# Kernel optimization log

Hardware: AMD Instinct MI355X
Metric: run time of the kernel (lower is better)

## Reference

```python
import jax, jax.numpy as jnp
import numpy as np

N = 500_000   # mesh vertices
M = 500_000   # non-manifold sample points
K = 4         # quad-mesh valence
WEIGHTS = [7000.0, 600.0, 10.0, 50.0, 30.0, 3.0]


def setup_inputs() -> dict:
    key = jax.random.key(0)
    ks = jax.random.split(key, 11)
    return {
        "manifold_pred": jax.random.normal(ks[0], (1, N), jnp.float32),
        "nonmanifold_pred": jax.random.normal(ks[1], (1, M), jnp.float32),
        "mnfld_grad": jax.random.normal(ks[2], (1, N, 3), jnp.float32),
        "nonmnfld_grad": jax.random.normal(ks[3], (1, M, 3), jnp.float32),
        "mnfld_hessian": jax.random.normal(ks[4], (1, N, 3, 3), jnp.float32),
        "mnfld_n_gt": jax.random.normal(ks[5], (1, N, 3), jnp.float32),
        "theta": jax.random.normal(ks[6], (1, N, 1), jnp.float32),
        "local_coord_u": jax.random.normal(ks[7], (1, N, 3), jnp.float32),
        "local_coord_v": jax.random.normal(ks[8], (1, N, 3), jnp.float32),
        "rot": jax.random.normal(ks[9], (N, K, 3, 3), jnp.float32),
        "neighbors": jax.random.randint(ks[10], (N, K), 0, N, jnp.int32),
    }


def reference(manifold_pred, nonmanifold_pred, mnfld_grad, nonmnfld_grad,
              mnfld_hessian, mnfld_n_gt, theta, local_coord_u, local_coord_v,
              rot, neighbors):
    H = mnfld_hessian[0]          # [N,3,3] per-vertex hessian
    n_gt = mnfld_n_gt[0]          # [N,3]

    # morse term: n^T H  (div_type == 'l1')
    morse = 0.5 * jnp.abs(jnp.einsum('nd,nde->ne', n_gt, H)).mean()

    sdf_term = jnp.abs(manifold_pred).mean()

    # eikonal over concatenated grads (morse path uses nonmnfld_grad when near_points is None)
    all_grads = jnp.concatenate([nonmnfld_grad, mnfld_grad], axis=-2)  # [1, M+N, 3]
    eikonal_term = jnp.abs(jnp.linalg.norm(all_grads, axis=2) - 1.0).mean()

    inter_term = jnp.exp(-100.0 * jnp.abs(nonmanifold_pred)).mean()

    # cross-field directions from theta
    u, v, th = local_coord_u[0], local_coord_v[0], theta[0]  # [N,3],[N,3],[N,1]
    va = u * jnp.cos(th) + v * jnp.sin(th)
    va = va / (jnp.linalg.norm(va, axis=-1, keepdims=True) + 1e-12)
    vb = -u * jnp.sin(th) + v * jnp.cos(th)
    vb = vb / (jnp.linalg.norm(vb, axis=-1, keepdims=True) + 1e-12)

    # per-vertex (v^T H) x v hessian alignment (single valence group covers all vertices)
    vaH = jnp.einsum('nd,nde->ne', va, H)
    vbH = jnp.einsum('nd,nde->ne', vb, H)
    h_alpha = jnp.abs(jnp.cross(vaH, va)).mean()
    h_beta = jnp.abs(jnp.cross(vbH, vb)).mean()
    theta_hessian_term = 0.5 * (h_alpha + h_beta)

    # neighbor consistency: rotate neighbor cross-field into vertex frame, dot products
    vaj = jnp.einsum('nkij,nkj->nki', rot, va[neighbors])  # [N,K,3]
    vbj = jnp.einsum('nkij,nkj->nki', rot, vb[neighbors])
    aa = jnp.abs(jnp.einsum('nd,nkd->nk', va, vaj))
    ab = jnp.abs(jnp.einsum('nd,nkd->nk', va, vbj))
    ba = jnp.abs(jnp.einsum('nd,nkd->nk', vb, vaj))
    bb = jnp.abs(jnp.einsum('nd,nkd->nk', vb, vbj))
    theta_neighbors_term = (aa + ab + ba + bb - 2.0).mean()

    w = WEIGHTS
    loss = (w[0] * sdf_term + w[1] * inter_term + w[3] * eikonal_term
            + w[5] * morse + w[2] * theta_hessian_term + w[4] * theta_neighbors_term)
    return jnp.stack([loss, sdf_term, inter_term, eikonal_term, morse,
                      theta_hessian_term, theta_neighbors_term])
```

## Files before the change

### kernel.cpp

```cpp
#include <hip/hip_runtime.h>
#include <math.h>

static constexpr int BLOCK = 256;
static constexpr int WAVES = BLOCK / 64;
static constexpr int KVAL = 4;
static constexpr int TILE = 256;

typedef float f4 __attribute__((ext_vector_type(4)));
typedef int i4 __attribute__((ext_vector_type(4)));
typedef unsigned int u4v __attribute__((ext_vector_type(4)));
union VV { u4v u4; _Float16 h[8]; };

__device__ __forceinline__ void nts4(u4v* p, u4v v) {
  __builtin_nontemporal_store(v, p);
}

__device__ __forceinline__ void norm3(float x, float y, float z,
                                      float& ox, float& oy, float& oz) {
  float inv = 1.0f / (sqrtf(x * x + y * y + z * z) + 1e-12f);
  ox = x * inv; oy = y * inv; oz = z * inv;
}

template <int NV>
__device__ __forceinline__ void block_reduce(float (&p)[NV]) {
#pragma unroll
  for (int off = 32; off > 0; off >>= 1)
#pragma unroll
    for (int q = 0; q < NV; ++q) p[q] += __shfl_down(p[q], off, 64);
  __shared__ float sm[WAVES][NV];
  int wave = threadIdx.x >> 6, lane = threadIdx.x & 63;
  if (lane == 0)
#pragma unroll
    for (int q = 0; q < NV; ++q) sm[wave][q] = p[q];
  __syncthreads();
  if (threadIdx.x == 0) {
#pragma unroll
    for (int q = 0; q < NV; ++q) {
      float t = 0.f;
#pragma unroll
      for (int w = 1; w < WAVES; ++w) t += sm[w][q];
      p[q] += t;
    }
  }
}

__device__ __forceinline__ void stage_f(float* __restrict__ dst,
                                        const float* __restrict__ src, int nf) {
  int t = threadIdx.x;
  int nf4 = nf >> 2;
  const f4* s4 = (const f4*)src;
  f4* d4 = (f4*)dst;
  for (int i = t; i < nf4; i += BLOCK) d4[i] = s4[i];
  int rem = nf & 3;
  if (t < rem) dst[nf4 * 4 + t] = src[nf4 * 4 + t];
}

__global__ __launch_bounds__(BLOCK) void s1_kernel(
    const float* __restrict__ theta, const float* __restrict__ u,
    const float* __restrict__ v, u4v* __restrict__ vavb, int N,
    const float* __restrict__ pred, const float* __restrict__ pgrad,
    const float* __restrict__ mp, const float* __restrict__ grad,
    const float* __restrict__ H, const float* __restrict__ ngt,
    float* __restrict__ part1, int nb1, int M) {
  __shared__ float B[2304];
  int t = threadIdx.x;
  long base = (long)blockIdx.x * TILE;
  float p[5] = {0.f, 0.f, 0.f, 0.f, 0.f};

  int cntM = 0, cntN = 0;
  if (base < M) { long c = (long)M - base; cntM = c > TILE ? TILE : (int)c; }
  if (base < N) { long c = (long)N - base; cntN = c > TILE ? TILE : (int)c; }

  float prv = 0.f, mpv = 0.f, thv = 0.f;
  if (t < cntM) prv = pred[base + t];
  if (t < cntN) { mpv = mp[base + t]; thv = theta[base + t]; }

  if (cntM > 0) stage_f(B, pgrad + 3 * base, 3 * cntM);
  __syncthreads();
  if (t < cntM) {
    float gx = B[3 * t], gy = B[3 * t + 1], gz = B[3 * t + 2];
    p[1] += fabsf(sqrtf(gx * gx + gy * gy + gz * gz) - 1.0f);
    p[4] += __expf(-100.0f * fabsf(prv));
  }
  __syncthreads();
  float ng0 = 0.f, ng1 = 0.f, ng2 = 0.f;
  if (cntN > 0) {
    stage_f(B, grad + 3 * base, 3 * cntN);
    stage_f(B + 768, ngt + 3 * base, 3 * cntN);
  }
  __syncthreads();
  if (t < cntN) {
    float gx = B[3 * t], gy = B[3 * t + 1], gz = B[3 * t + 2];
    p[1] += fabsf(sqrtf(gx * gx + gy * gy + gz * gz) - 1.0f);
    p[0] = fabsf(mpv);
    ng0 = B[768 + 3 * t]; ng1 = B[768 + 3 * t + 1]; ng2 = B[768 + 3 * t + 2];
  }
  __syncthreads();

  if (cntN > 0) {
    stage_f(B, u + 3 * base, 3 * cntN);
    stage_f(B + 768, v + 3 * base, 3 * cntN);
  }
  __syncthreads();
  float va[3] = {0.f, 0.f, 0.f}, vb[3] = {0.f, 0.f, 0.f};
  if (t < cntN) {
    float s, c;
    __sincosf(thv, &s, &c);
    float ux = B[3 * t], uy = B[3 * t + 1], uz = B[3 * t + 2];
    float vx = B[768 + 3 * t], vy = B[768 + 3 * t + 1], vz = B[768 + 3 * t + 2];
    norm3(ux * c + vx * s, uy * c + vy * s, uz * c + vz * s, va[0], va[1], va[2]);
    norm3(vx * c - ux * s, vy * c - uy * s, vz * c - uz * s, vb[0], vb[1], vb[2]);
    VV o;
    o.h[0] = (_Float16)va[0]; o.h[1] = (_Float16)va[1]; o.h[2] = (_Float16)va[2];
    o.h[3] = (_Float16)vb[0]; o.h[4] = (_Float16)vb[1]; o.h[5] = (_Float16)vb[2];
    o.h[6] = (_Float16)0.f;   o.h[7] = (_Float16)0.f;
    nts4(&vavb[base + t], o.u4);
  }
  __syncthreads();

  if (cntN > 0) stage_f(B, H + 9 * base, 9 * cntN);
  __syncthreads();
  if (t < cntN) {
    float h[9];
#pragma unroll
    for (int q = 0; q < 9; ++q) h[q] = B[9 * t + q];
    p[2] = fabsf(ng0 * h[0] + ng1 * h[3] + ng2 * h[6]) +
           fabsf(ng0 * h[1] + ng1 * h[4] + ng2 * h[7]) +
           fabsf(ng0 * h[2] + ng1 * h[5] + ng2 * h[8]);
    float a0 = va[0] * h[0] + va[1] * h[3] + va[2] * h[6];
    float a1 = va[0] * h[1] + va[1] * h[4] + va[2] * h[7];
    float a2 = va[0] * h[2] + va[1] * h[5] + va[2] * h[8];
    float b0 = vb[0] * h[0] + vb[1] * h[3] + vb[2] * h[6];
    float b1 = vb[0] * h[1] + vb[1] * h[4] + vb[2] * h[7];
    float b2 = vb[0] * h[2] + vb[1] * h[5] + vb[2] * h[8];
    p[3] = fabsf(a1 * va[2] - a2 * va[1]) + fabsf(a2 * va[0] - a0 * va[2]) +
           fabsf(a0 * va[1] - a1 * va[0]) + fabsf(b1 * vb[2] - b2 * vb[1]) +
           fabsf(b2 * vb[0] - b0 * vb[2]) + fabsf(b0 * vb[1] - b1 * vb[0]);
  }

  block_reduce<5>(p);
  if (t == 0) {
#pragma unroll
    for (int q = 0; q < 5; ++q) part1[q * nb1 + blockIdx.x] = p[q];
  }
}

__global__ __launch_bounds__(BLOCK) void s3_kernel(
    const u4v* __restrict__ vavb, const float* __restrict__ rot,
    const i4* __restrict__ nbr, float* __restrict__ part2, int N) {
  __shared__ float B[4608];
  int t = threadIdx.x;
  long base = (long)blockIdx.x * TILE;
  int cntN = 0;
  if (base < N) { long c = (long)N - base; cntN = c > TILE ? TILE : (int)c; }
  float p[1] = {0.f};

  VV wn[4]; VV ws;
  ws.u4 = u4v{0, 0, 0, 0};
#pragma unroll
  for (int k = 0; k < KVAL; ++k) wn[k].u4 = u4v{0, 0, 0, 0};
  if (t < cntN) {
    i4 jj = nbr[base + t];
    int js[4] = {jj.x, jj.y, jj.z, jj.w};
#pragma unroll
    for (int k = 0; k < KVAL; ++k) wn[k].u4 = vavb[js[k]];
    ws.u4 = vavb[base + t];
  }
  float va[3] = {(float)ws.h[0], (float)ws.h[1], (float)ws.h[2]};
  float vb[3] = {(float)ws.h[3], (float)ws.h[4], (float)ws.h[5]};

  float nsum = 0.f;
#pragma unroll
  for (int sp = 0; sp < 2; ++sp) {
    int cs = cntN - 128 * sp;
    if (cs < 0) cs = 0;
    if (cs > 128) cs = 128;
    if (cs > 0) stage_f(B, rot + 36 * (base + 128 * sp), 36 * cs);
    __syncthreads();
    int lt = t - 128 * sp;
    if (lt >= 0 && lt < cs) {
      const float* R0 = B + 36 * lt;
#pragma unroll
      for (int k = 0; k < KVAL; ++k) {
        float R[9];
#pragma unroll
        for (int q = 0; q < 9; ++q) R[q] = R0[9 * k + q];
        float pa0 = R[0] * va[0] + R[3] * va[1] + R[6] * va[2];
        float pa1 = R[1] * va[0] + R[4] * va[1] + R[7] * va[2];
        float pa2 = R[2] * va[0] + R[5] * va[1] + R[8] * va[2];
        float pb0 = R[0] * vb[0] + R[3] * vb[1] + R[6] * vb[2];
        float pb1 = R[1] * vb[0] + R[4] * vb[1] + R[7] * vb[2];
        float pb2 = R[2] * vb[0] + R[5] * vb[1] + R[8] * vb[2];
        float aj0 = (float)wn[k].h[0], aj1 = (float)wn[k].h[1],
              aj2 = (float)wn[k].h[2];
        float bj0 = (float)wn[k].h[3], bj1 = (float)wn[k].h[4],
              bj2 = (float)wn[k].h[5];
        nsum += fabsf(pa0 * aj0 + pa1 * aj1 + pa2 * aj2) +
                fabsf(pa0 * bj0 + pa1 * bj1 + pa2 * bj2) +
                fabsf(pb0 * aj0 + pb1 * aj1 + pb2 * aj2) +
                fabsf(pb0 * bj0 + pb1 * bj1 + pb2 * bj2) - 2.0f;
      }
    }
    __syncthreads();
  }
  p[0] = nsum;
  block_reduce<1>(p);
  if (t == 0) part2[blockIdx.x] = p[0];
}

__global__ __launch_bounds__(BLOCK) void finalize_fast(
    const float* __restrict__ part1, int nb1, const float* __restrict__ part2,
    int nb2, float* __restrict__ out, int N, int M) {
  float s[6] = {0.f, 0.f, 0.f, 0.f, 0.f, 0.f};
  for (int b = threadIdx.x; b < nb1; b += BLOCK) {
#pragma unroll
    for (int q = 0; q < 5; ++q) s[q] += part1[q * nb1 + b];
  }
  for (int b = threadIdx.x; b < nb2; b += BLOCK) s[5] += part2[b];
  block_reduce<6>(s);
  if (threadIdx.x == 0) {
    float sdf = s[0] / (float)N;
    float eik = s[1] / (float)(N + M);
    float morse = 0.5f * s[2] / (3.0f * (float)N);
    float th = 0.5f * s[3] / (3.0f * (float)N);
    float inter = s[4] / (float)M;
    float nb = s[5] / ((float)N * (float)KVAL);
    float loss = 7000.0f * sdf + 600.0f * inter + 50.0f * eik + 3.0f * morse +
                 10.0f * th + 30.0f * nb;
    out[0] = loss; out[1] = sdf; out[2] = inter; out[3] = eik;
    out[4] = morse; out[5] = th; out[6] = nb;
  }
}

__device__ __forceinline__ void crossfield(const float* __restrict__ u,
                                           const float* __restrict__ v,
                                           const float* __restrict__ theta,
                                           int n, float va[3], float vb[3]) {
  float s, c;
  __sincosf(theta[n], &s, &c);
  float ux = u[3 * n], uy = u[3 * n + 1], uz = u[3 * n + 2];
  float vx = v[3 * n], vy = v[3 * n + 1], vz = v[3 * n + 2];
  norm3(ux * c + vx * s, uy * c + vy * s, uz * c + vz * s, va[0], va[1], va[2]);
  norm3(vx * c - ux * s, vy * c - uy * s, vz * c - uz * s, vb[0], vb[1], vb[2]);
}

__global__ __launch_bounds__(BLOCK) void vertex_kernel(
    const float* __restrict__ mp, const float* __restrict__ grad,
    const float* __restrict__ H, const float* __restrict__ ngt,
    const float* __restrict__ theta, const float* __restrict__ u,
    const float* __restrict__ v, const float* __restrict__ rot,
    const int* __restrict__ nbr, float* __restrict__ acc, int N) {
  int n = blockIdx.x * blockDim.x + threadIdx.x;
  float p[5] = {0.f, 0.f, 0.f, 0.f, 0.f};
  if (n < N) {
    float hh[9];
#pragma unroll
    for (int i = 0; i < 9; ++i) hh[i] = H[9 * (size_t)n + i];
    p[0] = fabsf(mp[n]);
    float gx = grad[3 * n], gy = grad[3 * n + 1], gz = grad[3 * n + 2];
    p[1] = fabsf(sqrtf(gx * gx + gy * gy + gz * gz) - 1.0f);
    float n0 = ngt[3 * n], n1 = ngt[3 * n + 1], n2 = ngt[3 * n + 2];
    p[2] = fabsf(n0 * hh[0] + n1 * hh[3] + n2 * hh[6]) +
           fabsf(n0 * hh[1] + n1 * hh[4] + n2 * hh[7]) +
           fabsf(n0 * hh[2] + n1 * hh[5] + n2 * hh[8]);
    float va[3], vb[3];
    crossfield(u, v, theta, n, va, vb);
    {
      float a0 = va[0] * hh[0] + va[1] * hh[3] + va[2] * hh[6];
      float a1 = va[0] * hh[1] + va[1] * hh[4] + va[2] * hh[7];
      float a2 = va[0] * hh[2] + va[1] * hh[5] + va[2] * hh[8];
      float b0 = vb[0] * hh[0] + vb[1] * hh[3] + vb[2] * hh[6];
      float b1 = vb[0] * hh[1] + vb[1] * hh[4] + vb[2] * hh[7];
      float b2 = vb[0] * hh[2] + vb[1] * hh[5] + vb[2] * hh[8];
      p[3] = fabsf(a1 * va[2] - a2 * va[1]) + fabsf(a2 * va[0] - a0 * va[2]) +
             fabsf(a0 * va[1] - a1 * va[0]) + fabsf(b1 * vb[2] - b2 * vb[1]) +
             fabsf(b2 * vb[0] - b0 * vb[2]) + fabsf(b0 * vb[1] - b1 * vb[0]);
    }
    float nsum = 0.f;
    const float* R = rot + (size_t)n * (KVAL * 9);
#pragma unroll
    for (int k = 0; k < KVAL; ++k) {
      int j = nbr[KVAL * (size_t)n + k];
      float vaj[3], vbj[3];
      crossfield(u, v, theta, j, vaj, vbj);
      float r0 = R[9 * k + 0], r1 = R[9 * k + 1], r2 = R[9 * k + 2];
      float r3 = R[9 * k + 3], r4 = R[9 * k + 4], r5 = R[9 * k + 5];
      float r6 = R[9 * k + 6], r7 = R[9 * k + 7], r8 = R[9 * k + 8];
      float wa0 = r0 * vaj[0] + r1 * vaj[1] + r2 * vaj[2];
      float wa1 = r3 * vaj[0] + r4 * vaj[1] + r5 * vaj[2];
      float wa2 = r6 * vaj[0] + r7 * vaj[1] + r8 * vaj[2];
      float wb0 = r0 * vbj[0] + r1 * vbj[1] + r2 * vbj[2];
      float wb1 = r3 * vbj[0] + r4 * vbj[1] + r5 * vbj[2];
      float wb2 = r6 * vbj[0] + r7 * vbj[1] + r8 * vbj[2];
      nsum += fabsf(va[0] * wa0 + va[1] * wa1 + va[2] * wa2) +
              fabsf(va[0] * wb0 + va[1] * wb1 + va[2] * wb2) +
              fabsf(vb[0] * wa0 + vb[1] * wa1 + vb[2] * wa2) +
              fabsf(vb[0] * wb0 + vb[1] * wb1 + vb[2] * wb2) - 2.0f;
    }
    p[4] = nsum;
  }
  block_reduce<5>(p);
  if (threadIdx.x == 0) {
    atomicAdd(&acc[0], p[0]); atomicAdd(&acc[1], p[1]); atomicAdd(&acc[2], p[2]);
    atomicAdd(&acc[3], p[3]); atomicAdd(&acc[4], p[4]);
  }
}

__global__ __launch_bounds__(BLOCK) void point_kernel(
    const float* __restrict__ pred, const float* __restrict__ grad,
    float* __restrict__ acc, int M) {
  int i = blockIdx.x * blockDim.x + threadIdx.x;
  float p[2] = {0.f, 0.f};
  if (i < M) {
    p[0] = __expf(-100.0f * fabsf(pred[i]));
    float gx = grad[3 * i], gy = grad[3 * i + 1], gz = grad[3 * i + 2];
    p[1] = fabsf(sqrtf(gx * gx + gy * gy + gz * gz) - 1.0f);
  }
  block_reduce<2>(p);
  if (threadIdx.x == 0) {
    atomicAdd(&acc[5], p[0]); atomicAdd(&acc[1], p[1]);
  }
}

__global__ void finalize_acc(const float* __restrict__ acc, float* __restrict__ out,
                             int N, int M) {
  if (threadIdx.x == 0 && blockIdx.x == 0) {
    float sdf = acc[0] / (float)N;
    float eik = acc[1] / (float)(N + M);
    float morse = 0.5f * acc[2] / (3.0f * (float)N);
    float th = 0.5f * acc[3] / (3.0f * (float)N);
    float nb = acc[4] / ((float)N * (float)KVAL);
    float inter = acc[5] / (float)M;
    float loss = 7000.0f * sdf + 600.0f * inter + 50.0f * eik + 3.0f * morse +
                 10.0f * th + 30.0f * nb;
    out[0] = loss; out[1] = sdf; out[2] = inter; out[3] = eik;
    out[4] = morse; out[5] = th; out[6] = nb;
  }
}

extern "C" void kernel_launch(void* const* d_in, const int* in_sizes, int n_in,
                              void* d_out, int out_size, void* d_ws, size_t ws_size,
                              hipStream_t stream) {
  const float* mp    = (const float*)d_in[0];
  const float* npred = (const float*)d_in[1];
  const float* grad  = (const float*)d_in[2];
  const float* ngrad = (const float*)d_in[3];
  const float* H     = (const float*)d_in[4];
  const float* ngt   = (const float*)d_in[5];
  const float* theta = (const float*)d_in[6];
  const float* u     = (const float*)d_in[7];
  const float* v     = (const float*)d_in[8];
  const float* rot   = (const float*)d_in[9];
  const int*   nbr   = (const int*)d_in[10];
  float* out = (float*)d_out;

  int N = in_sizes[0];
  int M = in_sizes[1];
  int mx = (N > M) ? N : M;
  int nb1 = (mx + TILE - 1) / TILE;
  int nb2 = (N + TILE - 1) / TILE;

  size_t off_vavb = 256;
  size_t off_p1 = off_vavb + (size_t)N * 16;
  size_t off_p2 = off_p1 + (size_t)5 * nb1 * 4;
  size_t need = off_p2 + (size_t)nb2 * 4;

  if (ws_size >= need) {
    u4v* vavb    = (u4v*)((char*)d_ws + off_vavb);
    float* part1 = (float*)((char*)d_ws + off_p1);
    float* part2 = (float*)((char*)d_ws + off_p2);
    s1_kernel<<<nb1, BLOCK, 0, stream>>>(
        theta, u, v, vavb, N, npred, ngrad, mp, grad, H, ngt, part1, nb1, M);
    s3_kernel<<<nb2, BLOCK, 0, stream>>>(
        vavb, rot, (const i4*)nbr, part2, N);
    finalize_fast<<<1, BLOCK, 0, stream>>>(part1, nb1, part2, nb2, out, N, M);
  } else {
    float* acc = (float*)d_ws;
    (void)hipMemsetAsync(acc, 0, 6 * sizeof(float), stream);
    vertex_kernel<<<(N + BLOCK - 1) / BLOCK, BLOCK, 0, stream>>>(
        mp, grad, H, ngt, theta, u, v, rot, nbr, acc, N);
    point_kernel<<<(M + BLOCK - 1) / BLOCK, BLOCK, 0, stream>>>(npred, ngrad, acc, M);
    finalize_acc<<<1, 64, 0, stream>>>(acc, out, N, M);
  }
}
```

Before: 59.84 us.

## Split each vertex's neighbors across two threads and pad staged rot rows

The neighbor-consistency kernel now assigns two threads per vertex, each handling two of the four neighbors, so both halves of the tile run compute in each staging phase instead of half the block idling. The neighbor-index and vertex-data gathers are issued up front for both sub-tiles. Rotation matrices are staged into shared memory with a 37-float stride to avoid LDS bank conflicts. The cost is more gathers per thread (the own-vertex vavb load is duplicated across the pair) and integer division in the staging loop.

After: 59.77 us. No clear change (-0.1%).

```diff
diff --git a/kernel.cpp b/kernel.cpp
--- a/kernel.cpp
+++ b/kernel.cpp
@@ -8,6 +8,7 @@
 
 typedef float f4 __attribute__((ext_vector_type(4)));
 typedef int i4 __attribute__((ext_vector_type(4)));
+typedef int i2 __attribute__((ext_vector_type(2)));
 typedef unsigned int u4v __attribute__((ext_vector_type(4)));
 union VV { u4v u4; _Float16 h[8]; };
 
@@ -53,6 +54,19 @@
   for (int i = t; i < nf4; i += BLOCK) d4[i] = s4[i];
   int rem = nf & 3;
   if (t < rem) dst[nf4 * 4 + t] = src[nf4 * 4 + t];
+}
+
+__device__ __forceinline__ void stage_rot_pad(float* __restrict__ B,
+                                              const float* __restrict__ src,
+                                              int cs) {
+  int nf4 = 9 * cs;
+  const f4* s4 = (const f4*)src;
+  for (int i = threadIdx.x; i < nf4; i += BLOCK) {
+    f4 x = s4[i];
+    int vtx = i / 9, r = i - 9 * vtx;
+    float* d = B + vtx * 37 + r * 4;
+    d[0] = x.x; d[1] = x.y; d[2] = x.z; d[3] = x.w;
+  }
 }
 
 __global__ __launch_bounds__(BLOCK) void s1_kernel(
@@ -147,27 +161,30 @@
 
 __global__ __launch_bounds__(BLOCK) void s3_kernel(
     const u4v* __restrict__ vavb, const float* __restrict__ rot,
-    const i4* __restrict__ nbr, float* __restrict__ part2, int N) {
-  __shared__ float B[4608];
+    const i2* __restrict__ nbr2, float* __restrict__ part2, int N) {
+  __shared__ float B[128 * 37];
   int t = threadIdx.x;
+  int vl = t >> 1;
+  int h = t & 1;
   long base = (long)blockIdx.x * TILE;
   int cntN = 0;
   if (base < N) { long c = (long)N - base; cntN = c > TILE ? TILE : (int)c; }
-  float p[1] = {0.f};
-
-  VV wn[4]; VV ws;
-  ws.u4 = u4v{0, 0, 0, 0};
-#pragma unroll
-  for (int k = 0; k < KVAL; ++k) wn[k].u4 = u4v{0, 0, 0, 0};
-  if (t < cntN) {
-    i4 jj = nbr[base + t];
-    int js[4] = {jj.x, jj.y, jj.z, jj.w};
-#pragma unroll
-    for (int k = 0; k < KVAL; ++k) wn[k].u4 = vavb[js[k]];
-    ws.u4 = vavb[base + t];
-  }
-  float va[3] = {(float)ws.h[0], (float)ws.h[1], (float)ws.h[2]};
-  float vb[3] = {(float)ws.h[3], (float)ws.h[4], (float)ws.h[5]};
+
+  VV wn[2][2]; VV ws[2];
+#pragma unroll
+  for (int sp = 0; sp < 2; ++sp) {
+    ws[sp].u4 = u4v{0, 0, 0, 0};
+    wn[sp][0].u4 = u4v{0, 0, 0, 0};
+    wn[sp][1].u4 = u4v{0, 0, 0, 0};
+    int lv = 128 * sp + vl;
+    if (lv < cntN) {
+      long n = base + lv;
+      i2 jj = nbr2[2 * n + h];
+      wn[sp][0].u4 = vavb[jj.x];
+      wn[sp][1].u4 = vavb[jj.y];
+      ws[sp].u4 = vavb[n];
+    }
+  }
 
   float nsum = 0.f;
 #pragma unroll
@@ -175,13 +192,15 @@
     int cs = cntN - 128 * sp;
     if (cs < 0) cs = 0;
     if (cs > 128) cs = 128;
-    if (cs > 0) stage_f(B, rot + 36 * (base + 128 * sp), 36 * cs);
+    if (cs > 0) stage_rot_pad(B, rot + 36 * (base + 128 * sp), cs);
     __syncthreads();
-    int lt = t - 128 * sp;
-    if (lt >= 0 && lt < cs) {
-      const float* R0 = B + 36 * lt;
-#pragma unroll
-      for (int k = 0; k < KVAL; ++k) {
+    if (vl < cs) {
+      float va[3] = {(float)ws[sp].h[0], (float)ws[sp].h[1], (float)ws[sp].h[2]};
+      float vb[3] = {(float)ws[sp].h[3], (float)ws[sp].h[4], (float)ws[sp].h[5]};
+      const float* R0 = B + 37 * vl;
+#pragma unroll
+      for (int kk = 0; kk < 2; ++kk) {
+        int k = 2 * h + kk;
         float R[9];
 #pragma unroll
         for (int q = 0; q < 9; ++q) R[q] = R0[9 * k + q];
@@ -191,10 +210,10 @@
         float pb0 = R[0] * vb[0] + R[3] * vb[1] + R[6] * vb[2];
         float pb1 = R[1] * vb[0] + R[4] * vb[1] + R[7] * vb[2];
         float pb2 = R[2] * vb[0] + R[5] * vb[1] + R[8] * vb[2];
-        float aj0 = (float)wn[k].h[0], aj1 = (float)wn[k].h[1],
-              aj2 = (float)wn[k].h[2];
-        float bj0 = (float)wn[k].h[3], bj1 = (float)wn[k].h[4],
-              bj2 = (float)wn[k].h[5];
+        float aj0 = (float)wn[sp][kk].h[0], aj1 = (float)wn[sp][kk].h[1],
+              aj2 = (float)wn[sp][kk].h[2];
+        float bj0 = (float)wn[sp][kk].h[3], bj1 = (float)wn[sp][kk].h[4],
+              bj2 = (float)wn[sp][kk].h[5];
         nsum += fabsf(pa0 * aj0 + pa1 * aj1 + pa2 * aj2) +
                 fabsf(pa0 * bj0 + pa1 * bj1 + pa2 * bj2) +
                 fabsf(pb0 * aj0 + pb1 * aj1 + pb2 * aj2) +
@@ -203,7 +222,7 @@
     }
     __syncthreads();
   }
-  p[0] = nsum;
+  float p[1] = {nsum};
   block_reduce<1>(p);
   if (t == 0) part2[blockIdx.x] = p[0];
 }
@@ -372,7 +391,7 @@
     s1_kernel<<<nb1, BLOCK, 0, stream>>>(
         theta, u, v, vavb, N, npred, ngrad, mp, grad, H, ngt, part1, nb1, M);
     s3_kernel<<<nb2, BLOCK, 0, stream>>>(
-        vavb, rot, (const i4*)nbr, part2, N);
+        vavb, rot, (const i2*)nbr, part2, N);
     finalize_fast<<<1, BLOCK, 0, stream>>>(part1, nb1, part2, nb2, out, N, M);
   } else {
     float* acc = (float*)d_ws;
```
